# Optimization experiments

Hardware: AMD Instinct MI355X
Metric: run time of the kernel (lower is better)

Reference implementation:

```python
import jax, jax.numpy as jnp
import numpy as np
from jax import lax

DN = ('NCHW', 'OIHW', 'NCHW')

def _conv(x, w, dilation, pad):
    return lax.conv_general_dilated(x, w, window_strides=(1, 1),
                                    padding=((pad, pad), (pad, pad)),
                                    rhs_dilation=(dilation, dilation),
                                    dimension_numbers=DN)

def _avg_pool3(x):
    # 3x3 avg pool, stride 1, pad 1, count_include_pad=True (torch default)
    s = lax.reduce_window(x, 0.0, lax.add, (1, 1, 3, 3), (1, 1, 1, 1),
                          ((0, 0), (0, 0), (1, 1), (1, 1)))
    return s * (1.0 / 9.0)

def _max_pool3(x):
    return lax.reduce_window(x, -jnp.inf, lax.max, (1, 1, 3, 3), (1, 1, 1, 1),
                             ((0, 0), (0, 0), (1, 1), (1, 1)))

def _mixed_op(h, w3, wd3, alpha):
    # softmax-weighted sum of 5 candidate ops (DARTS mixed edge)
    a = jax.nn.softmax(alpha, axis=-1)
    return (a[0] * h
            + a[1] * _conv(h, w3, 1, 1)
            + a[2] * _conv(h, wd3, 2, 2)
            + a[3] * _avg_pool3(h)
            + a[4] * _max_pool3(h))

def setup_inputs() -> dict:
    key = jax.random.key(0)
    ks = jax.random.split(key, 8)
    B, C, H, W = 64, 128, 32, 32
    return {
        'input0': jax.random.normal(ks[0], (B, C, H, W), jnp.float32),
        'input1': jax.random.normal(ks[1], (B, C, H, W), jnp.float32),
        'skip_input': jax.random.normal(ks[2], (B, C, H, W), jnp.float32),
        'w_pre0': jax.random.normal(ks[3], (C, C, 1, 1), jnp.float32) * 0.05,
        'w_pre1': jax.random.normal(ks[4], (C, C, 1, 1), jnp.float32) * 0.05,
        'w_conv3': jax.random.normal(ks[5], (8, C, C, 3, 3), jnp.float32) * 0.05,
        'w_dil3': jax.random.normal(ks[6], (8, C, C, 3, 3), jnp.float32) * 0.05,
        'alphas': jnp.full((8, 5), 1.0 / 5.0, jnp.float32),
    }

def reference(input0, input1, skip_input, w_pre0, w_pre1, w_conv3, w_dil3, alphas):
    node_num = 4
    s0 = _conv(input0, w_pre0, 1, 0)   # preprocess0: 1x1 conv C_prev_prev -> C
    s1 = _conv(input1, w_pre1, 1, 0)   # preprocess1: 1x1 conv C_prev -> C
    states = [s0, s1]
    offset = 0
    for i in range(node_num):
        h0, h1 = states[-2], states[-1]
        s = (_mixed_op(h0, w_conv3[offset], w_dil3[offset], alphas[offset])
             + _mixed_op(h1, w_conv3[offset + 1], w_dil3[offset + 1], alphas[offset + 1]))
        states.append(s)
        offset += 2
    states.append(skip_input)
    out = jnp.concatenate(states[-(node_num + 1):], axis=1)  # [B, 5C, H, W]
    return (out, skip_input)
```

## Files before the change

kernel.cpp:

```cpp
#include <hip/hip_runtime.h>
#include <math.h>

#define B    64
#define C    128
#define H    32
#define W    32
#define HW   1024
#define OUTC 640
#define PS   37
#define NSKIP (B*C*HW)
#define NW    (8*C*C*9)

#define ALPHA_OFF 0
#define S0_OFF    64
#define S1_OFF    (S0_OFF + NSKIP)
#define W3_OFF    (S1_OFF + NSKIP)
#define WD3_OFF   (W3_OFF + NW)

__global__ __launch_bounds__(256) void prep_kernel(
    const float* __restrict__ alphas, const float* __restrict__ w3,
    const float* __restrict__ wd3, float* __restrict__ ws) {
  __shared__ float as[40];
  int tid = threadIdx.x;
  if (tid < 8) {
    float v[5];
    float m = -1e30f;
    for (int j = 0; j < 5; j++) { v[j] = alphas[tid * 5 + j]; m = fmaxf(m, v[j]); }
    float s = 0.f;
    for (int j = 0; j < 5; j++) { v[j] = __expf(v[j] - m); s += v[j]; }
    float inv = 1.f / s;
    for (int j = 0; j < 5; j++) as[tid * 5 + j] = v[j] * inv;
  }
  __syncthreads();
  if (blockIdx.x == 0 && tid < 40) ws[ALPHA_OFF + tid] = as[tid];
  int stride = gridDim.x * blockDim.x;
  for (int i = blockIdx.x * blockDim.x + tid; i < 2 * NW; i += stride) {
    if (i < NW) {
      int o = i / (C * C * 9);
      ws[W3_OFF + i] = as[o * 5 + 1] * w3[i];
    } else {
      int j = i - NW;
      int o = j / (C * C * 9);
      ws[WD3_OFF + j] = as[o * 5 + 2] * wd3[j];
    }
  }
}

__global__ __launch_bounds__(256) void pre_kernel(
    const float* __restrict__ in0, const float* __restrict__ in1,
    const float* __restrict__ wp0, const float* __restrict__ wp1,
    float* __restrict__ ws) {
  int which = blockIdx.z;
  const float* in = which ? in1 : in0;
  const float* wp = which ? wp1 : wp0;
  float* out = ws + (which ? S1_OFF : S0_OFF);
  int b = blockIdx.x;
  int cg = blockIdx.y;
  int t = threadIdx.x;
  int hw0 = t * 4;

  float4 acc[16];
  #pragma unroll
  for (int k = 0; k < 16; k++) acc[k] = make_float4(0.f, 0.f, 0.f, 0.f);

  const float* ip = in + b * (C * HW) + hw0;
  #pragma unroll 4
  for (int ci = 0; ci < C; ci++) {
    float4 x = *(const float4*)(ip + ci * HW);
    #pragma unroll
    for (int k = 0; k < 16; k++) {
      float wv = wp[(cg * 16 + k) * C + ci];
      acc[k].x += wv * x.x; acc[k].y += wv * x.y;
      acc[k].z += wv * x.z; acc[k].w += wv * x.w;
    }
  }
  #pragma unroll
  for (int k = 0; k < 16; k++)
    *(float4*)(out + b * (C * HW) + (cg * 16 + k) * HW + hw0) = acc[k];
}

__global__ __launch_bounds__(256) void node_kernel(
    const float* __restrict__ h0, int h0_bs,
    const float* __restrict__ h1, int h1_bs,
    const float* __restrict__ ws, int o0,
    float* __restrict__ out) {
  __shared__ float p0[PS * PS];
  __shared__ float p1[PS * PS];

  int b = blockIdx.x;
  int cog = blockIdx.y;
  int tid = threadIdx.x;
  int y = tid >> 3;
  int x0 = (tid & 7) * 4;

  float a0_0 = ws[ALPHA_OFF + o0 * 5 + 0];
  float a3_0 = ws[ALPHA_OFF + o0 * 5 + 3];
  float a4_0 = ws[ALPHA_OFF + o0 * 5 + 4];
  float a0_1 = ws[ALPHA_OFF + (o0 + 1) * 5 + 0];
  float a3_1 = ws[ALPHA_OFF + (o0 + 1) * 5 + 3];
  float a4_1 = ws[ALPHA_OFF + (o0 + 1) * 5 + 4];

  const float* w3_e0 = ws + W3_OFF  + o0 * (C * C * 9);
  const float* wd_e0 = ws + WD3_OFF + o0 * (C * C * 9);
  const float* w3_e1 = w3_e0 + (C * C * 9);
  const float* wd_e1 = wd_e0 + (C * C * 9);

  const float* h0b = h0 + b * h0_bs;
  const float* h1b = h1 + b * h1_bs;

  float acc[8][4];
  #pragma unroll
  for (int c = 0; c < 8; c++)
    #pragma unroll
    for (int k = 0; k < 4; k++) acc[c][k] = 0.f;

  for (int ci = 0; ci < C; ci++) {
    for (int j = tid; j < PS * PS; j += 256) {
      int py = j / PS, px = j - py * PS;
      int yy = py - 2, xx = px - 2;
      bool v = (yy >= 0) & (yy < H) & (xx >= 0) & (xx < W);
      int off = ci * HW + yy * W + xx;
      p0[j] = v ? h0b[off] : 0.f;
      p1[j] = v ? h1b[off] : 0.f;
    }
    __syncthreads();

    int cidx = ci - cog * 8;
    if (cidx >= 0 && cidx < 8) {
      #pragma unroll
      for (int k = 0; k < 4; k++) {
        int x = x0 + k;
        int pc = (y + 2) * PS + (x + 2);
        {
          float cen = p0[pc];
          float s9 = 0.f;
          #pragma unroll
          for (int dy = -1; dy <= 1; dy++)
            #pragma unroll
            for (int dx = -1; dx <= 1; dx++) s9 += p0[pc + dy * PS + dx];
          float mx = cen;
          #pragma unroll
          for (int dy = -1; dy <= 1; dy++)
            #pragma unroll
            for (int dx = -1; dx <= 1; dx++) {
              int yy = y + dy, xx = x + dx;
              if (yy >= 0 && yy < H && xx >= 0 && xx < W)
                mx = fmaxf(mx, p0[pc + dy * PS + dx]);
            }
          acc[cidx][k] += a0_0 * cen + a3_0 * (s9 * (1.f / 9.f)) + a4_0 * mx;
        }
        {
          float cen = p1[pc];
          float s9 = 0.f;
          #pragma unroll
          for (int dy = -1; dy <= 1; dy++)
            #pragma unroll
            for (int dx = -1; dx <= 1; dx++) s9 += p1[pc + dy * PS + dx];
          float mx = cen;
          #pragma unroll
          for (int dy = -1; dy <= 1; dy++)
            #pragma unroll
            for (int dx = -1; dx <= 1; dx++) {
              int yy = y + dy, xx = x + dx;
              if (yy >= 0 && yy < H && xx >= 0 && xx < W)
                mx = fmaxf(mx, p1[pc + dy * PS + dx]);
            }
          acc[cidx][k] += a0_1 * cen + a3_1 * (s9 * (1.f / 9.f)) + a4_1 * mx;
        }
      }
    }

    float A1[3][6], A2[3][8], B1[3][6], B2[3][8];
    #pragma unroll
    for (int r = 0; r < 3; r++)
      #pragma unroll
      for (int c = 0; c < 6; c++) {
        A1[r][c] = p0[(y + 1 + r) * PS + x0 + 1 + c];
        B1[r][c] = p1[(y + 1 + r) * PS + x0 + 1 + c];
      }
    #pragma unroll
    for (int r = 0; r < 3; r++)
      #pragma unroll
      for (int c = 0; c < 8; c++) {
        A2[r][c] = p0[(y + 2 * r) * PS + x0 + c];
        B2[r][c] = p1[(y + 2 * r) * PS + x0 + c];
      }

    #pragma unroll
    for (int c = 0; c < 8; c++) {
      int co = cog * 8 + c;
      const float* pw3_0 = w3_e0 + (co * C + ci) * 9;
      const float* pwd_0 = wd_e0 + (co * C + ci) * 9;
      const float* pw3_1 = w3_e1 + (co * C + ci) * 9;
      const float* pwd_1 = wd_e1 + (co * C + ci) * 9;
      #pragma unroll
      for (int t = 0; t < 9; t++) {
        int ky = t / 3, kx = t - ky * 3;
        float w3a = pw3_0[t], wda = pwd_0[t];
        float w3b = pw3_1[t], wdb = pwd_1[t];
        #pragma unroll
        for (int k = 0; k < 4; k++) {
          acc[c][k] += w3a * A1[ky][k + kx];
          acc[c][k] += wda * A2[ky][k + 2 * kx];
          acc[c][k] += w3b * B1[ky][k + kx];
          acc[c][k] += wdb * B2[ky][k + 2 * kx];
        }
      }
    }
    __syncthreads();
  }

  #pragma unroll
  for (int c = 0; c < 8; c++) {
    float* op = out + b * (OUTC * HW) + (cog * 8 + c) * HW + y * W + x0;
    *(float4*)op = make_float4(acc[c][0], acc[c][1], acc[c][2], acc[c][3]);
  }
}

__global__ __launch_bounds__(256) void skip_kernel(
    const float* __restrict__ skip, float* __restrict__ dout) {
  int i = blockIdx.x * 256 + threadIdx.x;
  if (i < NSKIP / 4) {
    float4 v = ((const float4*)skip)[i];
    int e = i * 4;
    int b = e >> 17;
    int rem = e & (C * HW - 1);
    *(float4*)(dout + b * (OUTC * HW) + 512 * HW + rem) = v;
    *(float4*)(dout + B * (OUTC * HW) + e) = v;
  }
}

extern "C" void kernel_launch(void* const* d_in, const int* in_sizes, int n_in,
                              void* d_out, int out_size, void* d_ws, size_t ws_size,
                              hipStream_t stream) {
  const float* input0 = (const float*)d_in[0];
  const float* input1 = (const float*)d_in[1];
  const float* skip   = (const float*)d_in[2];
  const float* wpre0  = (const float*)d_in[3];
  const float* wpre1  = (const float*)d_in[4];
  const float* wconv3 = (const float*)d_in[5];
  const float* wdil3  = (const float*)d_in[6];
  const float* alphas = (const float*)d_in[7];
  float* out = (float*)d_out;
  float* ws  = (float*)d_ws;

  prep_kernel<<<512, 256, 0, stream>>>(alphas, wconv3, wdil3, ws);
  pre_kernel<<<dim3(B, 8, 2), 256, 0, stream>>>(input0, input1, wpre0, wpre1, ws);

  const float* s0 = ws + S0_OFF;
  const float* s1 = ws + S1_OFF;
  const int wsb = C * HW;
  const int ob  = OUTC * HW;

  node_kernel<<<dim3(B, 16), 256, 0, stream>>>(s0, wsb, s1, wsb, ws, 0, out + 0 * C * HW);
  node_kernel<<<dim3(B, 16), 256, 0, stream>>>(s1, wsb, out + 0 * C * HW, ob, ws, 2, out + 1 * C * HW);
  node_kernel<<<dim3(B, 16), 256, 0, stream>>>(out + 0 * C * HW, ob, out + 1 * C * HW, ob, ws, 4, out + 2 * C * HW);
  node_kernel<<<dim3(B, 16), 256, 0, stream>>>(out + 1 * C * HW, ob, out + 2 * C * HW, ob, ws, 6, out + 3 * C * HW);

  skip_kernel<<<(NSKIP / 4 + 255) / 256, 256, 0, stream>>>(skip, out);
}
```

Before: 6.265 ms.

## Give each wavefront a private double-buffered LDS row band, removing block barriers

The node kernel no longer stages a full padded 37x37 plane per input channel behind two block-wide barriers. Each wavefront now owns a 12-row band (8 rows plus 2-row halos) in LDS, double-buffered across input channels. The next channel is prefetched from global into registers while the current one is computed, so no __syncthreads is needed inside the channel loop. The convolution is reorganized row by row with vectorized LDS reads and pooling fused into the same row loads. This trades more LDS and registers, and relies on intra-wavefront ordering for correctness, to remove barrier stalls and redundant padded-plane loads.

Result: slower. 11.27 ms (+79.9%).

```diff
diff --git a/kernel.cpp b/kernel.cpp
--- a/kernel.cpp
+++ b/kernel.cpp
@@ -7,9 +7,12 @@
 #define W    32
 #define HW   1024
 #define OUTC 640
-#define PS   37
 #define NSKIP (B*C*HW)
 #define NW    (8*C*C*9)
+
+#define BRS   40
+#define BROWS 12
+#define BPLANE (BROWS*BRS)
 
 #define ALPHA_OFF 0
 #define S0_OFF    64
@@ -84,14 +87,16 @@
     const float* __restrict__ h1, int h1_bs,
     const float* __restrict__ ws, int o0,
     float* __restrict__ out) {
-  __shared__ float p0[PS * PS];
-  __shared__ float p1[PS * PS];
+  __shared__ float band[4][2][2][BPLANE];
 
   int b = blockIdx.x;
   int cog = blockIdx.y;
   int tid = threadIdx.x;
-  int y = tid >> 3;
-  int x0 = (tid & 7) * 4;
+  int wv = tid >> 6;
+  int l  = tid & 63;
+  int ly = l >> 3;
+  int x0 = (l & 7) * 4;
+  int y  = wv * 8 + ly;
 
   float a0_0 = ws[ALPHA_OFF + o0 * 5 + 0];
   float a3_0 = ws[ALPHA_OFF + o0 * 5 + 3];
@@ -105,8 +110,43 @@
   const float* w3_e1 = w3_e0 + (C * C * 9);
   const float* wd_e1 = wd_e0 + (C * C * 9);
 
-  const float* h0b = h0 + b * h0_bs;
-  const float* h1b = h1 + b * h1_bs;
+  const float* gi0 = h0 + b * h0_bs + y * W + x0;
+  const float* gi1 = h1 + b * h1_bs + y * W + x0;
+
+  bool top  = (l < 16);
+  int  hp   = (l >> 3) & 1;
+  int  hrow = top ? (wv * 8 - 2 + hp) : (wv * 8 + 8 + hp);
+  bool hval = (l < 32) && (top ? (wv > 0) : (wv < 3));
+  int  hcol = (l & 7) * 4;
+  int  hrc  = hrow < 0 ? 0 : (hrow > 31 ? 31 : hrow);
+  const float* gh0 = h0 + b * h0_bs + hrc * W + hcol;
+  const float* gh1 = h1 + b * h1_bs + hrc * W + hcol;
+  int hwo = (top ? hp : 10 + hp) * BRS + hcol + 2;
+  int wo  = (ly + 2) * BRS + x0 + 2;
+
+  {
+    float* zb = &band[0][0][0][0];
+    for (int j = tid; j < 4 * 2 * 2 * BPLANE; j += 256) zb[j] = 0.f;
+  }
+  __syncthreads();
+
+  float* b00 = &band[wv][0][0][0];
+  float* b01 = &band[wv][0][1][0];
+  float* b10 = &band[wv][1][0][0];
+  float* b11 = &band[wv][1][1][0];
+
+  {
+    float4 ia = *(const float4*)gi0;
+    float4 ib = *(const float4*)gi1;
+    b00[wo] = ia.x; b00[wo+1] = ia.y; b00[wo+2] = ia.z; b00[wo+3] = ia.w;
+    b01[wo] = ib.x; b01[wo+1] = ib.y; b01[wo+2] = ib.z; b01[wo+3] = ib.w;
+    if (hval) {
+      float4 ha = *(const float4*)gh0;
+      float4 hb = *(const float4*)gh1;
+      b00[hwo] = ha.x; b00[hwo+1] = ha.y; b00[hwo+2] = ha.z; b00[hwo+3] = ha.w;
+      b01[hwo] = hb.x; b01[hwo+1] = hb.y; b01[hwo+2] = hb.z; b01[hwo+3] = hb.w;
+    }
+  }
 
   float acc[8][4];
   #pragma unroll
@@ -114,100 +154,209 @@
     #pragma unroll
     for (int k = 0; k < 4; k++) acc[c][k] = 0.f;
 
-  for (int ci = 0; ci < C; ci++) {
-    for (int j = tid; j < PS * PS; j += 256) {
-      int py = j / PS, px = j - py * PS;
-      int yy = py - 2, xx = px - 2;
-      bool v = (yy >= 0) & (yy < H) & (xx >= 0) & (xx < W);
-      int off = ci * HW + yy * W + xx;
-      p0[j] = v ? h0b[off] : 0.f;
-      p1[j] = v ? h1b[off] : 0.f;
-    }
-    __syncthreads();
-
+  bool ru = (y >= 1), rd = (y <= 30);
+
+  auto compute_ci = [&](int ci, const float* p0, const float* p1) {
     int cidx = ci - cog * 8;
-    if (cidx >= 0 && cidx < 8) {
+    bool dopool = (cidx >= 0) & (cidx < 8);
+    float cenA[4], cenB[4], s9A[4], s9B[4], mxA[4], mxB[4];
+    int wq = (cog * 8 * C + ci) * 9;
+
+    {
+      const float* rp0 = p0 + ly * BRS + x0;
+      const float* rp1 = p1 + ly * BRS + x0;
+      float Ra[8], Rb[8];
+      *(float4*)&Ra[0] = *(const float4*)(rp0);
+      *(float4*)&Ra[4] = *(const float4*)(rp0 + 4);
+      *(float4*)&Rb[0] = *(const float4*)(rp1);
+      *(float4*)&Rb[4] = *(const float4*)(rp1 + 4);
+      #pragma unroll
+      for (int c = 0; c < 8; c++) {
+        int wi = wq + c * (C * 9);
+        #pragma unroll
+        for (int kx = 0; kx < 3; kx++) {
+          float wa = wd_e0[wi + kx], wb = wd_e1[wi + kx];
+          #pragma unroll
+          for (int k = 0; k < 4; k++) {
+            acc[c][k] += wa * Ra[k + 2 * kx];
+            acc[c][k] += wb * Rb[k + 2 * kx];
+          }
+        }
+      }
+    }
+    {
+      const float* rp0 = p0 + (ly + 1) * BRS + x0;
+      const float* rp1 = p1 + (ly + 1) * BRS + x0;
+      float Ra[8], Rb[8];
+      *(float4*)&Ra[0] = *(const float4*)(rp0);
+      *(float4*)&Ra[4] = *(const float4*)(rp0 + 4);
+      *(float4*)&Rb[0] = *(const float4*)(rp1);
+      *(float4*)&Rb[4] = *(const float4*)(rp1 + 4);
+      #pragma unroll
+      for (int c = 0; c < 8; c++) {
+        int wi = wq + c * (C * 9);
+        #pragma unroll
+        for (int kx = 0; kx < 3; kx++) {
+          float wa = w3_e0[wi + kx], wb = w3_e1[wi + kx];
+          #pragma unroll
+          for (int k = 0; k < 4; k++) {
+            acc[c][k] += wa * Ra[k + kx + 1];
+            acc[c][k] += wb * Rb[k + kx + 1];
+          }
+        }
+      }
+      if (dopool) {
+        #pragma unroll
+        for (int k = 0; k < 4; k++) {
+          s9A[k] = Ra[k+1] + Ra[k+2] + Ra[k+3];
+          s9B[k] = Rb[k+1] + Rb[k+2] + Rb[k+3];
+          float ma = -1e30f, mb = -1e30f;
+          if (ru) {
+            if (x0 + k >= 1)  { ma = fmaxf(ma, Ra[k+1]); mb = fmaxf(mb, Rb[k+1]); }
+            ma = fmaxf(ma, Ra[k+2]); mb = fmaxf(mb, Rb[k+2]);
+            if (x0 + k <= 30) { ma = fmaxf(ma, Ra[k+3]); mb = fmaxf(mb, Rb[k+3]); }
+          }
+          mxA[k] = ma; mxB[k] = mb;
+        }
+      }
+    }
+    {
+      const float* rp0 = p0 + (ly + 2) * BRS + x0;
+      const float* rp1 = p1 + (ly + 2) * BRS + x0;
+      float Ra[8], Rb[8];
+      *(float4*)&Ra[0] = *(const float4*)(rp0);
+      *(float4*)&Ra[4] = *(const float4*)(rp0 + 4);
+      *(float4*)&Rb[0] = *(const float4*)(rp1);
+      *(float4*)&Rb[4] = *(const float4*)(rp1 + 4);
+      #pragma unroll
+      for (int c = 0; c < 8; c++) {
+        int wi = wq + c * (C * 9);
+        #pragma unroll
+        for (int kx = 0; kx < 3; kx++) {
+          float wa = wd_e0[wi + 3 + kx], wb = wd_e1[wi + 3 + kx];
+          #pragma unroll
+          for (int k = 0; k < 4; k++) {
+            acc[c][k] += wa * Ra[k + 2 * kx];
+            acc[c][k] += wb * Rb[k + 2 * kx];
+          }
+        }
+        #pragma unroll
+        for (int kx = 0; kx < 3; kx++) {
+          float wa = w3_e0[wi + 3 + kx], wb = w3_e1[wi + 3 + kx];
+          #pragma unroll
+          for (int k = 0; k < 4; k++) {
+            acc[c][k] += wa * Ra[k + kx + 1];
+            acc[c][k] += wb * Rb[k + kx + 1];
+          }
+        }
+      }
+      if (dopool) {
+        #pragma unroll
+        for (int k = 0; k < 4; k++) {
+          s9A[k] += Ra[k+1] + Ra[k+2] + Ra[k+3];
+          s9B[k] += Rb[k+1] + Rb[k+2] + Rb[k+3];
+          cenA[k] = Ra[k+2]; cenB[k] = Rb[k+2];
+          float ma = mxA[k], mb = mxB[k];
+          if (x0 + k >= 1)  { ma = fmaxf(ma, Ra[k+1]); mb = fmaxf(mb, Rb[k+1]); }
+          ma = fmaxf(ma, Ra[k+2]); mb = fmaxf(mb, Rb[k+2]);
+          if (x0 + k <= 30) { ma = fmaxf(ma, Ra[k+3]); mb = fmaxf(mb, Rb[k+3]); }
+          mxA[k] = ma; mxB[k] = mb;
+        }
+      }
+    }
+    {
+      const float* rp0 = p0 + (ly + 3) * BRS + x0;
+      const float* rp1 = p1 + (ly + 3) * BRS + x0;
+      float Ra[8], Rb[8];
+      *(float4*)&Ra[0] = *(const float4*)(rp0);
+      *(float4*)&Ra[4] = *(const float4*)(rp0 + 4);
+      *(float4*)&Rb[0] = *(const float4*)(rp1);
+      *(float4*)&Rb[4] = *(const float4*)(rp1 + 4);
+      #pragma unroll
+      for (int c = 0; c < 8; c++) {
+        int wi = wq + c * (C * 9);
+        #pragma unroll
+        for (int kx = 0; kx < 3; kx++) {
+          float wa = w3_e0[wi + 6 + kx], wb = w3_e1[wi + 6 + kx];
+          #pragma unroll
+          for (int k = 0; k < 4; k++) {
+            acc[c][k] += wa * Ra[k + kx + 1];
+            acc[c][k] += wb * Rb[k + kx + 1];
+          }
+        }
+      }
+      if (dopool) {
+        #pragma unroll
+        for (int k = 0; k < 4; k++) {
+          s9A[k] += Ra[k+1] + Ra[k+2] + Ra[k+3];
+          s9B[k] += Rb[k+1] + Rb[k+2] + Rb[k+3];
+          float ma = mxA[k], mb = mxB[k];
+          if (rd) {
+            if (x0 + k >= 1)  { ma = fmaxf(ma, Ra[k+1]); mb = fmaxf(mb, Rb[k+1]); }
+            ma = fmaxf(ma, Ra[k+2]); mb = fmaxf(mb, Rb[k+2]);
+            if (x0 + k <= 30) { ma = fmaxf(ma, Ra[k+3]); mb = fmaxf(mb, Rb[k+3]); }
+          }
+          mxA[k] = ma; mxB[k] = mb;
+        }
+      }
+    }
+    {
+      const float* rp0 = p0 + (ly + 4) * BRS + x0;
+      const float* rp1 = p1 + (ly + 4) * BRS + x0;
+      float Ra[8], Rb[8];
+      *(float4*)&Ra[0] = *(const float4*)(rp0);
+      *(float4*)&Ra[4] = *(const float4*)(rp0 + 4);
+      *(float4*)&Rb[0] = *(const float4*)(rp1);
+      *(float4*)&Rb[4] = *(const float4*)(rp1 + 4);
+      #pragma unroll
+      for (int c = 0; c < 8; c++) {
+        int wi = wq + c * (C * 9);
+        #pragma unroll
+        for (int kx = 0; kx < 3; kx++) {
+          float wa = wd_e0[wi + 6 + kx], wb = wd_e1[wi + 6 + kx];
+          #pragma unroll
+          for (int k = 0; k < 4; k++) {
+            acc[c][k] += wa * Ra[k + 2 * kx];
+            acc[c][k] += wb * Rb[k + 2 * kx];
+          }
+        }
+      }
+    }
+    if (dopool) {
       #pragma unroll
       for (int k = 0; k < 4; k++) {
-        int x = x0 + k;
-        int pc = (y + 2) * PS + (x + 2);
-        {
-          float cen = p0[pc];
-          float s9 = 0.f;
-          #pragma unroll
-          for (int dy = -1; dy <= 1; dy++)
-            #pragma unroll
-            for (int dx = -1; dx <= 1; dx++) s9 += p0[pc + dy * PS + dx];
-          float mx = cen;
-          #pragma unroll
-          for (int dy = -1; dy <= 1; dy++)
-            #pragma unroll
-            for (int dx = -1; dx <= 1; dx++) {
-              int yy = y + dy, xx = x + dx;
-              if (yy >= 0 && yy < H && xx >= 0 && xx < W)
-                mx = fmaxf(mx, p0[pc + dy * PS + dx]);
-            }
-          acc[cidx][k] += a0_0 * cen + a3_0 * (s9 * (1.f / 9.f)) + a4_0 * mx;
-        }
-        {
-          float cen = p1[pc];
-          float s9 = 0.f;
-          #pragma unroll
-          for (int dy = -1; dy <= 1; dy++)
-            #pragma unroll
-            for (int dx = -1; dx <= 1; dx++) s9 += p1[pc + dy * PS + dx];
-          float mx = cen;
-          #pragma unroll
-          for (int dy = -1; dy <= 1; dy++)
-            #pragma unroll
-            for (int dx = -1; dx <= 1; dx++) {
-              int yy = y + dy, xx = x + dx;
-              if (yy >= 0 && yy < H && xx >= 0 && xx < W)
-                mx = fmaxf(mx, p1[pc + dy * PS + dx]);
-            }
-          acc[cidx][k] += a0_1 * cen + a3_1 * (s9 * (1.f / 9.f)) + a4_1 * mx;
-        }
-      }
-    }
-
-    float A1[3][6], A2[3][8], B1[3][6], B2[3][8];
-    #pragma unroll
-    for (int r = 0; r < 3; r++)
-      #pragma unroll
-      for (int c = 0; c < 6; c++) {
-        A1[r][c] = p0[(y + 1 + r) * PS + x0 + 1 + c];
-        B1[r][c] = p1[(y + 1 + r) * PS + x0 + 1 + c];
-      }
-    #pragma unroll
-    for (int r = 0; r < 3; r++)
-      #pragma unroll
-      for (int c = 0; c < 8; c++) {
-        A2[r][c] = p0[(y + 2 * r) * PS + x0 + c];
-        B2[r][c] = p1[(y + 2 * r) * PS + x0 + c];
-      }
-
-    #pragma unroll
-    for (int c = 0; c < 8; c++) {
-      int co = cog * 8 + c;
-      const float* pw3_0 = w3_e0 + (co * C + ci) * 9;
-      const float* pwd_0 = wd_e0 + (co * C + ci) * 9;
-      const float* pw3_1 = w3_e1 + (co * C + ci) * 9;
-      const float* pwd_1 = wd_e1 + (co * C + ci) * 9;
-      #pragma unroll
-      for (int t = 0; t < 9; t++) {
-        int ky = t / 3, kx = t - ky * 3;
-        float w3a = pw3_0[t], wda = pwd_0[t];
-        float w3b = pw3_1[t], wdb = pwd_1[t];
-        #pragma unroll
-        for (int k = 0; k < 4; k++) {
-          acc[c][k] += w3a * A1[ky][k + kx];
-          acc[c][k] += wda * A2[ky][k + 2 * kx];
-          acc[c][k] += w3b * B1[ky][k + kx];
-          acc[c][k] += wdb * B2[ky][k + 2 * kx];
-        }
-      }
-    }
-    __syncthreads();
+        acc[cidx][k] += a0_0 * cenA[k] + a3_0 * (s9A[k] * (1.f / 9.f)) + a4_0 * mxA[k];
+        acc[cidx][k] += a0_1 * cenB[k] + a3_1 * (s9B[k] * (1.f / 9.f)) + a4_1 * mxB[k];
+      }
+    }
+  };
+
+  auto step = [&](int ci, const float* r0, const float* r1, float* w0, float* w1) {
+    float4 ia = make_float4(0.f, 0.f, 0.f, 0.f), ib = ia, ha = ia, hb = ia;
+    bool pf = (ci + 1 < C);
+    if (pf) {
+      ia = *(const float4*)(gi0 + (ci + 1) * HW);
+      ib = *(const float4*)(gi1 + (ci + 1) * HW);
+      if (hval) {
+        ha = *(const float4*)(gh0 + (ci + 1) * HW);
+        hb = *(const float4*)(gh1 + (ci + 1) * HW);
+      }
+    }
+    __builtin_amdgcn_sched_barrier(0);
+    compute_ci(ci, r0, r1);
+    if (pf) {
+      w0[wo] = ia.x; w0[wo+1] = ia.y; w0[wo+2] = ia.z; w0[wo+3] = ia.w;
+      w1[wo] = ib.x; w1[wo+1] = ib.y; w1[wo+2] = ib.z; w1[wo+3] = ib.w;
+      if (hval) {
+        w0[hwo] = ha.x; w0[hwo+1] = ha.y; w0[hwo+2] = ha.z; w0[hwo+3] = ha.w;
+        w1[hwo] = hb.x; w1[hwo+1] = hb.y; w1[hwo+2] = hb.z; w1[hwo+3] = hb.w;
+      }
+    }
+  };
+
+  for (int ci = 0; ci < C; ci += 2) {
+    step(ci,     b00, b01, b10, b11);
+    step(ci + 1, b10, b11, b00, b01);
   }
 
   #pragma unroll
```
